# Kernel optimization log

Measured on AMD Instinct MI355X. Metric: run time of the kernel, lower is better.

The kernel has to match this reference:

```python
import jax, jax.numpy as jnp
import numpy as np

B, T, D = 2, 2048, 1024
NH, DH = 16, 64  # inner = NH*DH = D
SCALE_INIT = 0.02


def setup_inputs() -> dict:
    key = jax.random.key(0)
    kx, kq, kk, kv, ko = jax.random.split(key, 5)
    return {
        "x": jax.random.normal(kx, (B, T, D), dtype=jnp.float32),
        "Wq": jax.random.normal(kq, (D, NH * DH), dtype=jnp.float32) * SCALE_INIT,
        "Wk": jax.random.normal(kk, (D, NH * DH), dtype=jnp.float32) * SCALE_INIT,
        "Wv": jax.random.normal(kv, (D, NH * DH), dtype=jnp.float32) * SCALE_INIT,
        "Wo": jax.random.normal(ko, (NH * DH, D), dtype=jnp.float32) * SCALE_INIT,
    }


def reference(x, Wq, Wk, Wv, Wo):
    # x: (B, T, D)
    b, t, _ = x.shape

    def split_heads(h):
        # (B, T, NH*DH) -> (B, NH, T, DH)
        return h.reshape(b, t, NH, DH).transpose(0, 2, 1, 3)

    q = split_heads(x @ Wq)
    k = split_heads(x @ Wk)
    v = split_heads(x @ Wv)

    scale = jnp.asarray(1.0 / np.sqrt(DH), dtype=x.dtype)
    # The per-chunk loop in the original is mathematically equivalent to
    # full causal attention: each query row attends to keys with k_pos <= q_pos.
    scores = jnp.einsum("bhqd,bhkd->bhqk", q, k) * scale  # (B, NH, T, T)
    causal_mask = jnp.arange(t)[None, :] > jnp.arange(t)[:, None]  # k_pos > q_pos
    scores = jnp.where(causal_mask, -jnp.inf, scores)
    attn = jax.nn.softmax(scores, axis=-1)
    attn = jnp.nan_to_num(attn)  # matches torch.nan_to_num (no fully-masked rows in causal case)
    o = jnp.einsum("bhqk,bhkd->bhqd", attn, v)  # (B, NH, T, DH)
    o = o.transpose(0, 2, 1, 3).reshape(b, t, NH * DH)  # merge heads
    return o @ Wo  # (B, T, D)
```

## Files before the change

kernel.cpp:

```cpp
#include <hip/hip_runtime.h>
#include <hip/hip_bf16.h>
#include <string.h>

#define Bsz 2
#define Tsz 2048
#define Dsz 1024
#define NHsz 16
#define Msz (Bsz*Tsz)

typedef unsigned short bfu;
typedef __attribute__((ext_vector_type(8))) short short8;
typedef __attribute__((ext_vector_type(4))) short short4v;
typedef __attribute__((ext_vector_type(4))) float floatx4;

__device__ __forceinline__ bfu f2bf(float f) {
  unsigned int u = __builtin_bit_cast(unsigned int, f);
  u += 0x7fffu + ((u >> 16) & 1u);
  return (bfu)(u >> 16);
}

__device__ __forceinline__ float fexp2(float x) {
#if __has_builtin(__builtin_amdgcn_exp2f)
  return __builtin_amdgcn_exp2f(x);
#else
  return exp2f(x);
#endif
}

__device__ __forceinline__ short4v pack4bf(float a, float b, float c_, float d) {
  __hip_bfloat162 h01 = __float22bfloat162_rn(make_float2(a, b));
  __hip_bfloat162 h23 = __float22bfloat162_rn(make_float2(c_, d));
  uint2 uu;
  memcpy(&uu.x, &h01, 4);
  memcpy(&uu.y, &h23, 4);
  return __builtin_bit_cast(short4v, uu);
}

__device__ __forceinline__ short8 pack8bf(float4 a, float4 b) {
  __hip_bfloat162 h0 = __float22bfloat162_rn(make_float2(a.x, a.y));
  __hip_bfloat162 h1 = __float22bfloat162_rn(make_float2(a.z, a.w));
  __hip_bfloat162 h2 = __float22bfloat162_rn(make_float2(b.x, b.y));
  __hip_bfloat162 h3 = __float22bfloat162_rn(make_float2(b.z, b.w));
  uint4 u;
  memcpy(&u.x, &h0, 4); memcpy(&u.y, &h1, 4);
  memcpy(&u.z, &h2, 4); memcpy(&u.w, &h3, 4);
  return __builtin_bit_cast(short8, u);
}

__device__ __forceinline__ void async16(const void* g, void* l) {
  void* gnc = (void*)g;
  __builtin_amdgcn_global_load_lds((__attribute__((address_space(1))) void*)gnc,
                                   (__attribute__((address_space(3))) void*)l,
                                   16, 0, 0);
}

__global__ __launch_bounds__(256) void xcvt(const float* __restrict__ x, bfu* __restrict__ xb) {
  const size_t i = ((size_t)blockIdx.x * 256 + threadIdx.x) * 8;
  float4 a = *(const float4*)(x + i);
  float4 b = *(const float4*)(x + i + 4);
  *(short8*)(xb + i) = pack8bf(a, b);
}

__global__ __launch_bounds__(256) void transpose_w(const float* __restrict__ W0, const float* __restrict__ W1,
                                                   const float* __restrict__ W2, const float* __restrict__ W3,
                                                   bfu* __restrict__ wt) {
  __shared__ float tile[32][33];
  const float* W = blockIdx.z == 0 ? W0 : blockIdx.z == 1 ? W1 : blockIdx.z == 2 ? W2 : W3;
  const float s = (blockIdx.z == 0) ? 0.18033688011112042f : 1.0f;
  bfu* WT = wt + (size_t)blockIdx.z * Dsz * Dsz;
  int tx = threadIdx.x, ty = threadIdx.y;
  int kb = blockIdx.y * 32, nb = blockIdx.x * 32;
#pragma unroll
  for (int i = 0; i < 4; ++i)
    tile[ty + i*8][tx] = W[(size_t)(kb + ty + i*8) * Dsz + nb + tx];
  __syncthreads();
#pragma unroll
  for (int i = 0; i < 4; ++i)
    WT[(size_t)(nb + ty + i*8) * Dsz + kb + tx] = f2bf(tile[tx][ty + i*8] * s);
}

template <bool F32OUT, int NT>
__global__ __launch_bounds__(256) void gemm128(const bfu* __restrict__ Ain, const bfu* __restrict__ Bt0,
                                               void* __restrict__ C0, int K, int N,
                                               size_t strideB, size_t strideC) {
  constexpr int NJ = NT / 32;
  const int tid = threadIdx.x, wave = tid >> 6, lane = tid & 63;
  const int g = lane >> 4, c = lane & 15;
  const int m0 = blockIdx.y * 128, n0 = blockIdx.x * NT;
  const bfu* Bt = Bt0 + strideB * blockIdx.z;
  __shared__ bfu smem[4096 + NT * 32];
  bfu* As = smem;
  bfu* Bs = smem + 4096;
  floatx4 acc[4][NJ] = {};
  const int srow = lane >> 2, scol = (lane & 3) * 8;
  const bfu* gB = Bt + (size_t)(n0 + srow) * K + scol;
  const int wm = (wave >> 1) * 64, wn = (wave & 1) * (NT / 2);
  const bfu* gA = Ain + (size_t)(m0 + srow) * K + scol;

  for (int k0 = 0; k0 < K; k0 += 32) {
    __syncthreads();
#pragma unroll
    for (int cc = 0; cc < 2; ++cc) {
      const int chunk = wave * 2 + cc;
      async16(gA + (size_t)chunk * 16 * K + k0, &As[chunk * 512]);
    }
#pragma unroll
    for (int cc = 0; cc < NT/64; ++cc) {
      const int chunk = wave * (NT/64) + cc;
      async16(gB + (size_t)chunk * 16 * K + k0, &Bs[chunk * 512]);
    }
    __syncthreads();
    short8 afr[4], bfr[NJ];
#pragma unroll
    for (int t = 0; t < 4; ++t) afr[t] = *(const short8*)&As[(wm + t*16 + c) * 32 + g * 8];
#pragma unroll
    for (int t = 0; t < NJ; ++t) bfr[t] = *(const short8*)&Bs[(wn + t*16 + c) * 32 + g * 8];
#pragma unroll
    for (int i = 0; i < 4; ++i)
#pragma unroll
      for (int j = 0; j < NJ; ++j)
        acc[i][j] = __builtin_amdgcn_mfma_f32_16x16x32_bf16(afr[i], bfr[j], acc[i][j], 0, 0, 0);
  }

  const bool vtrans = (!F32OUT) && (NT == 128) && (blockIdx.z == 2);
  if (vtrans) {
    bfu* vtp = (bfu*)C0 + (size_t)2 * strideC;
#pragma unroll
    for (int p = 0; p < 2; ++p) {
      __syncthreads();
      if ((wave & 1) == p) {
#pragma unroll
        for (int i = 0; i < 4; ++i)
#pragma unroll
          for (int j = 0; j < NJ; ++j) {
            const int nl = j*16 + c;
            const int mg = ((wm + i*16) >> 3) + (g >> 1);
            const int phys = nl * 128 + ((mg ^ (nl & 15)) << 3) + ((g & 1) << 2);
            *(short4v*)&smem[phys] = pack4bf(acc[i][j][0], acc[i][j][1],
                                             acc[i][j][2], acc[i][j][3]);
          }
      }
      __syncthreads();
      const int h_ = (n0 + p * 64) >> 6;
      bfu* dst = vtp + ((size_t)((m0 >> 11) * 16 + h_) * 64) * Tsz + (m0 & 2047);
#pragma unroll
      for (int s = 0; s < 4; ++s) {
        const int nl = s * 16 + (tid >> 4);
        const int me = (tid & 15) << 3;
        const int phys = nl * 128 + (((me >> 3) ^ (nl & 15)) << 3);
        *(short8*)&dst[(size_t)nl * Tsz + me] = *(const short8*)&smem[phys];
      }
    }
    return;
  }

#pragma unroll
  for (int i = 0; i < 4; ++i) {
#pragma unroll
    for (int j = 0; j < NJ; ++j) {
      const int m = m0 + wm + i*16 + g*4;
      const int n = n0 + wn + j*16 + c;
#pragma unroll
      for (int r = 0; r < 4; ++r) {
        float v = acc[i][j][r];
        if (F32OUT) ((float*)C0)[(size_t)(m + r) * N + n] = v;
        else        ((bfu*)C0)[strideC * blockIdx.z + (size_t)(m + r) * N + n] = f2bf(v);
      }
    }
  }
}

__global__ __launch_bounds__(256, 4) void attn_kernel(const bfu* __restrict__ qkv,
                                                      float* __restrict__ op0,
                                                      float* __restrict__ op1,
                                                      float2* __restrict__ ml) {
  const int tid = threadIdx.x, wave = tid >> 6, lane = tid & 63;
  const int g = (lane >> 4) & 3, c = lane & 15, c7 = c & 7;

  const int flat = (int)blockIdx.y * 32 + (int)blockIdx.x;
  const int xcd = flat & 7, r_ = flat >> 3;
  const int ksplit = r_ & 1;
  const int s = (r_ >> 1) & 3, j0 = r_ >> 3;
  const int bh = xcd * 4 + s;
  const int b = bh >> 4, h = bh & 15;

  const size_t hbq = (size_t)b * Tsz * Dsz + h * 64;
  const bfu* Qp = qkv + hbq;
  const bfu* Kp = qkv + (size_t)Msz * Dsz + hbq;
  const bfu* Vt = qkv + (size_t)2 * Msz * Dsz + (size_t)bh * 64 * Tsz;
  float* op = ksplit ? op1 : op0;

  __shared__ bfu Ks[2][64 * 64];
  __shared__ bfu Vs[2][64 * 64];

  const int srow8 = lane >> 3;
  const int soff = ((lane & 7) ^ srow8) << 3;
  const floatx4 z4 = {0.0f, 0.0f, 0.0f, 0.0f};

  for (int hf = 0; hf < 2; ++hf) {
    const int j = hf ? (31 - j0) : j0;
    const int qw = j * 64 + wave * 16;

    short8 bq[2];
#pragma unroll
    for (int kk = 0; kk < 2; ++kk)
      bq[kk] = *(const short8*)(Qp + (size_t)(qw + c) * Dsz + kk * 32 + g * 8);

    floatx4 acc[4] = {};
    float mi = -3.0e38f, li = 0.0f;

    if (ksplit <= j) {
      const bfu* kpp[2]; const bfu* vpp[2];
#pragma unroll
      for (int cc = 0; cc < 2; ++cc) {
        const int ch = wave * 2 + cc;
        kpp[cc] = Kp + (size_t)(ksplit * 64 + ch * 8 + srow8) * Dsz + soff;
        vpp[cc] = Vt + (size_t)(ch * 8 + srow8) * Tsz + ksplit * 64 + soff;
      }

#pragma unroll
      for (int cc = 0; cc < 2; ++cc) {
        const int ch = wave * 2 + cc;
        async16(kpp[cc], &Ks[0][ch * 512]);
        async16(vpp[cc], &Vs[0][ch * 512]);
        kpp[cc] += (size_t)128 * Dsz;
        vpp[cc] += 128;
      }

      int cur = 0;
      for (int kt = ksplit; kt <= j; kt += 2) {
        if (kt + 2 <= j) {
#pragma unroll
          for (int cc = 0; cc < 2; ++cc) {
            const int ch = wave * 2 + cc;
            async16(kpp[cc], &Ks[cur ^ 1][ch * 512]);
            async16(vpp[cc], &Vs[cur ^ 1][ch * 512]);
            kpp[cc] += (size_t)128 * Dsz;
            vpp[cc] += 128;
          }
          asm volatile("s_waitcnt vmcnt(4)" ::: "memory");
        } else {
          asm volatile("s_waitcnt vmcnt(0)" ::: "memory");
        }
        __builtin_amdgcn_s_barrier();
        asm volatile("" ::: "memory");

        const bfu* KsC = &Ks[cur][0];
        const bfu* VsC = &Vs[cur][0];

        floatx4 st[4];
        __builtin_amdgcn_s_setprio(1);
#pragma unroll
        for (int mk = 0; mk < 4; ++mk) {
          const short8 kf = *(const short8*)&KsC[(mk * 16 + c) * 64 + ((g ^ c7) << 3)];
          st[mk] = __builtin_amdgcn_mfma_f32_16x16x32_bf16(kf, bq[0], z4, 0, 0, 0);
        }
#pragma unroll
        for (int mk = 0; mk < 4; ++mk) {
          const short8 kf = *(const short8*)&KsC[(mk * 16 + c) * 64 + (((4 + g) ^ c7) << 3)];
          st[mk] = __builtin_amdgcn_mfma_f32_16x16x32_bf16(kf, bq[1], st[mk], 0, 0, 0);
        }
        __builtin_amdgcn_s_setprio(0);

        if (kt == j) {
#pragma unroll
          for (int mk = 0; mk < 4; ++mk) {
            const int keyb = kt * 64 + mk * 16 + g * 4;
#pragma unroll
            for (int r = 0; r < 4; ++r)
              if (keyb + r > qw + c) st[mk][r] = -1.0e38f;
          }
        }

        float mloc = -3.0e38f;
#pragma unroll
        for (int mk = 0; mk < 4; ++mk)
          mloc = fmaxf(mloc, fmaxf(fmaxf(st[mk][0], st[mk][1]),
                                   fmaxf(st[mk][2], st[mk][3])));
        const bool resc = !__all(mloc <= mi + 8.0f);
        if (resc) {
          float mr = fmaxf(mloc, __shfl_xor(mloc, 16));
          mr = fmaxf(mr, __shfl_xor(mr, 32));
          const float mnew = fmaxf(mi, mr);
          const float alpha = fexp2(mi - mnew);
          li *= alpha;
          mi = mnew;
          float al[4];
#pragma unroll
          for (int rr = 0; rr < 4; ++rr) al[rr] = __shfl(alpha, (lane & 48) | (g * 4 + rr));
#pragma unroll
          for (int nd = 0; nd < 4; ++nd)
#pragma unroll
            for (int rr = 0; rr < 4; ++rr) acc[nd][rr] *= al[rr];
        }
        short4v pa[4];
#pragma unroll
        for (int mk = 0; mk < 4; ++mk) {
          const float p0 = fexp2(st[mk][0] - mi);
          const float p1 = fexp2(st[mk][1] - mi);
          const float p2 = fexp2(st[mk][2] - mi);
          const float p3 = fexp2(st[mk][3] - mi);
          li += (p0 + p1) + (p2 + p3);
          pa[mk] = pack4bf(p0, p1, p2, p3);
        }

        __builtin_amdgcn_s_setprio(1);
#pragma unroll
        for (int mk = 0; mk < 4; ++mk)
#pragma unroll
          for (int nd = 0; nd < 4; ++nd) {
            const short4v vf = *(const short4v*)&VsC[(nd * 16 + c) * 64 +
                ((((mk << 1) + (g >> 1)) ^ c7) << 3) + ((g & 1) << 2)];
            acc[nd] = __builtin_amdgcn_mfma_f32_16x16x16bf16_1k(pa[mk], vf, acc[nd], 0, 0, 0);
          }
        __builtin_amdgcn_s_setprio(0);

        asm volatile("" ::: "memory");
        __builtin_amdgcn_s_barrier();
        asm volatile("" ::: "memory");
        cur ^= 1;
      }
    }

    float lt = li;
    lt += __shfl_xor(lt, 16);
    lt += __shfl_xor(lt, 32);
#pragma unroll
    for (int rr = 0; rr < 4; ++rr) {
      const float lr = __shfl(lt, (lane & 48) | (g * 4 + rr));
      const float inv = lr > 0.0f ? 1.0f / lr : 0.0f;
#pragma unroll
      for (int nd = 0; nd < 4; ++nd)
        op[(size_t)(b * Tsz + qw + g * 4 + rr) * Dsz + h * 64 + nd * 16 + c] =
            acc[nd][rr] * inv;
    }
    if (lane < 16)
      ml[(size_t)ksplit * 65536 + bh * 2048 + qw + c] = make_float2(mi, lt);
  }
}

__global__ __launch_bounds__(256) void merge_split(const float* __restrict__ o0,
                                                   const float* __restrict__ o1,
                                                   const float2* __restrict__ ml,
                                                   bfu* __restrict__ ob) {
  const int idx = blockIdx.x * 256 + threadIdx.x;
  const int row = idx >> 7, ch = idx & 127;
  const int b = row >> 11, q = row & 2047;
  const int bh = b * 16 + (ch >> 3);
  const float2 a0 = ml[bh * 2048 + q];
  const float2 a1 = ml[65536 + bh * 2048 + q];
  const float M = fmaxf(a0.x, a1.x);
  const float w0 = fexp2(a0.x - M) * a0.y;
  const float w1 = fexp2(a1.x - M) * a1.y;
  const float inv = 1.0f / (w0 + w1);
  const float u0 = w0 * inv, u1 = w1 * inv;
  const size_t off = (size_t)row * 1024 + ch * 8;
  float4 p0 = *(const float4*)(o0 + off), q0 = *(const float4*)(o0 + off + 4);
  float4 p1 = *(const float4*)(o1 + off), q1 = *(const float4*)(o1 + off + 4);
  float4 ra, rb;
  ra.x = u0*p0.x + u1*p1.x; ra.y = u0*p0.y + u1*p1.y;
  ra.z = u0*p0.z + u1*p1.z; ra.w = u0*p0.w + u1*p1.w;
  rb.x = u0*q0.x + u1*q1.x; rb.y = u0*q0.y + u1*q1.y;
  rb.z = u0*q0.z + u1*q1.z; rb.w = u0*q0.w + u1*q1.w;
  *(short8*)(ob + off) = pack8bf(ra, rb);
}

extern "C" void kernel_launch(void* const* d_in, const int* in_sizes, int n_in,
                              void* d_out, int out_size, void* d_ws, size_t ws_size,
                              hipStream_t stream) {
  const float* x  = (const float*)d_in[0];
  const float* Wq = (const float*)d_in[1];
  const float* Wk = (const float*)d_in[2];
  const float* Wv = (const float*)d_in[3];
  const float* Wo = (const float*)d_in[4];
  float* out = (float*)d_out;

  bfu* wt    = (bfu*)d_ws;
  bfu* qkv   = wt + (size_t)4 * Dsz * Dsz;
  bfu* obuf  = qkv + (size_t)3 * Msz * Dsz;
  float* op0 = (float*)(obuf + (size_t)Msz * Dsz);
  float* op1 = op0 + (size_t)Msz * Dsz;
  float2* ml = (float2*)(op1 + (size_t)Msz * Dsz);

  transpose_w<<<dim3(32, 32, 4), dim3(32, 8), 0, stream>>>(Wq, Wk, Wv, Wo, wt);
  xcvt<<<dim3(2048), dim3(256), 0, stream>>>(x, obuf);
  gemm128<false, 128><<<dim3(Dsz / 128, Msz / 128, 3), dim3(256), 0, stream>>>(
      obuf, wt, (void*)qkv, Dsz, Dsz, (size_t)Dsz * Dsz, (size_t)Msz * Dsz);
  attn_kernel<<<dim3(32, 32), dim3(256), 0, stream>>>(qkv, op0, op1, ml);
  merge_split<<<dim3(2048), dim3(256), 0, stream>>>(op0, op1, ml, obuf);
  gemm128<true, 64><<<dim3(Dsz / 64, Msz / 128, 1), dim3(256), 0, stream>>>(
      obuf, wt + (size_t)3 * Dsz * Dsz, (void*)out, Dsz, Dsz,
      (size_t)0, (size_t)0);
}
```

Before: 195.9 us.

## Double-buffer GEMM LDS staging with XOR swizzle and fold x conversion into transpose

The bf16 GEMM now keeps two LDS stage buffers and issues the async global-to-LDS loads for the next K step before computing the current one. It waits on vmcnt so the copy overlaps the MFMA work, where before each step loaded and then computed in series. The 16-byte column chunks are XOR-swizzled on both the write and read side to cut LDS bank conflicts. The separate x-to-bf16 conversion kernel becomes an extra z-slice of the weight transpose launch, saving one kernel launch. The costs are doubled LDS per block, which may lower occupancy, and hand-tuned vmcnt counts that must match the number of outstanding loads.

```diff
diff --git a/kernel.cpp b/kernel.cpp
--- a/kernel.cpp
+++ b/kernel.cpp
@@ -54,16 +54,19 @@
                                    16, 0, 0);
 }
 
-__global__ __launch_bounds__(256) void xcvt(const float* __restrict__ x, bfu* __restrict__ xb) {
-  const size_t i = ((size_t)blockIdx.x * 256 + threadIdx.x) * 8;
-  float4 a = *(const float4*)(x + i);
-  float4 b = *(const float4*)(x + i + 4);
-  *(short8*)(xb + i) = pack8bf(a, b);
-}
-
 __global__ __launch_bounds__(256) void transpose_w(const float* __restrict__ W0, const float* __restrict__ W1,
                                                    const float* __restrict__ W2, const float* __restrict__ W3,
-                                                   bfu* __restrict__ wt) {
+                                                   bfu* __restrict__ wt,
+                                                   const float* __restrict__ x, bfu* __restrict__ xb) {
+  if (blockIdx.z == 4) {
+    const int bf = (int)blockIdx.y * 32 + (int)blockIdx.x;
+    const size_t i = ((size_t)bf * 256 + threadIdx.y * 32 + threadIdx.x) * 16;
+    float4 a0 = *(const float4*)(x + i),     a1 = *(const float4*)(x + i + 4);
+    float4 b0 = *(const float4*)(x + i + 8), b1 = *(const float4*)(x + i + 12);
+    *(short8*)(xb + i)     = pack8bf(a0, a1);
+    *(short8*)(xb + i + 8) = pack8bf(b0, b1);
+    return;
+  }
   __shared__ float tile[32][33];
   const float* W = blockIdx.z == 0 ? W0 : blockIdx.z == 1 ? W1 : blockIdx.z == 2 ? W2 : W3;
   const float s = (blockIdx.z == 0) ? 0.18033688011112042f : 1.0f;
@@ -88,42 +91,65 @@
   const int g = lane >> 4, c = lane & 15;
   const int m0 = blockIdx.y * 128, n0 = blockIdx.x * NT;
   const bfu* Bt = Bt0 + strideB * blockIdx.z;
-  __shared__ bfu smem[4096 + NT * 32];
-  bfu* As = smem;
-  bfu* Bs = smem + 4096;
+  __shared__ bfu smem[2][4096 + NT * 32];
   floatx4 acc[4][NJ] = {};
-  const int srow = lane >> 2, scol = (lane & 3) * 8;
+  const int srow = lane >> 2;
+  const int scol = (((lane & 3) ^ ((lane >> 3) & 3)) << 3);
   const bfu* gB = Bt + (size_t)(n0 + srow) * K + scol;
+  const bfu* gA = Ain + (size_t)(m0 + srow) * K + scol;
   const int wm = (wave >> 1) * 64, wn = (wave & 1) * (NT / 2);
-  const bfu* gA = Ain + (size_t)(m0 + srow) * K + scol;
-
-  for (int k0 = 0; k0 < K; k0 += 32) {
-    __syncthreads();
-#pragma unroll
-    for (int cc = 0; cc < 2; ++cc) {
-      const int chunk = wave * 2 + cc;
-      async16(gA + (size_t)chunk * 16 * K + k0, &As[chunk * 512]);
+  const int roct = (g ^ ((c >> 1) & 3)) << 3;
+
+#define STAGE_G(buf, k0)                                                        \
+  {                                                                             \
+    _Pragma("unroll")                                                           \
+    for (int cc = 0; cc < 2; ++cc) {                                            \
+      const int chunk = wave * 2 + cc;                                          \
+      async16(gA + (size_t)chunk * 16 * K + (k0), &smem[buf][chunk * 512]);     \
+    }                                                                           \
+    _Pragma("unroll")                                                           \
+    for (int cc = 0; cc < NT / 64; ++cc) {                                      \
+      const int chunk = wave * (NT / 64) + cc;                                  \
+      async16(gB + (size_t)chunk * 16 * K + (k0), &smem[buf][4096 + chunk * 512]); \
+    }                                                                           \
+  }
+
+  const int NK = K / 32;
+  STAGE_G(0, 0);
+  for (int t = 0; t < NK; ++t) {
+    const int cur = t & 1;
+    if (t + 1 < NK) {
+      STAGE_G(cur ^ 1, (t + 1) * 32);
+      if (NT == 128) asm volatile("s_waitcnt vmcnt(4)" ::: "memory");
+      else           asm volatile("s_waitcnt vmcnt(3)" ::: "memory");
+    } else {
+      asm volatile("s_waitcnt vmcnt(0)" ::: "memory");
     }
-#pragma unroll
-    for (int cc = 0; cc < NT/64; ++cc) {
-      const int chunk = wave * (NT/64) + cc;
-      async16(gB + (size_t)chunk * 16 * K + k0, &Bs[chunk * 512]);
-    }
-    __syncthreads();
+    __builtin_amdgcn_s_barrier();
+    asm volatile("" ::: "memory");
+
+    const bfu* AsC = &smem[cur][0];
+    const bfu* BsC = &smem[cur][4096];
     short8 afr[4], bfr[NJ];
 #pragma unroll
-    for (int t = 0; t < 4; ++t) afr[t] = *(const short8*)&As[(wm + t*16 + c) * 32 + g * 8];
-#pragma unroll
-    for (int t = 0; t < NJ; ++t) bfr[t] = *(const short8*)&Bs[(wn + t*16 + c) * 32 + g * 8];
+    for (int i = 0; i < 4; ++i) afr[i] = *(const short8*)&AsC[(wm + i*16 + c) * 32 + roct];
+#pragma unroll
+    for (int j = 0; j < NJ; ++j) bfr[j] = *(const short8*)&BsC[(wn + j*16 + c) * 32 + roct];
 #pragma unroll
     for (int i = 0; i < 4; ++i)
 #pragma unroll
       for (int j = 0; j < NJ; ++j)
         acc[i][j] = __builtin_amdgcn_mfma_f32_16x16x32_bf16(afr[i], bfr[j], acc[i][j], 0, 0, 0);
-  }
+
+    asm volatile("" ::: "memory");
+    __builtin_amdgcn_s_barrier();
+    asm volatile("" ::: "memory");
+  }
+#undef STAGE_G
 
   const bool vtrans = (!F32OUT) && (NT == 128) && (blockIdx.z == 2);
   if (vtrans) {
+    bfu* sm = &smem[0][0];
     bfu* vtp = (bfu*)C0 + (size_t)2 * strideC;
 #pragma unroll
     for (int p = 0; p < 2; ++p) {
@@ -136,8 +162,8 @@
             const int nl = j*16 + c;
             const int mg = ((wm + i*16) >> 3) + (g >> 1);
             const int phys = nl * 128 + ((mg ^ (nl & 15)) << 3) + ((g & 1) << 2);
-            *(short4v*)&smem[phys] = pack4bf(acc[i][j][0], acc[i][j][1],
-                                             acc[i][j][2], acc[i][j][3]);
+            *(short4v*)&sm[phys] = pack4bf(acc[i][j][0], acc[i][j][1],
+                                           acc[i][j][2], acc[i][j][3]);
           }
       }
       __syncthreads();
@@ -148,7 +174,7 @@
         const int nl = s * 16 + (tid >> 4);
         const int me = (tid & 15) << 3;
         const int phys = nl * 128 + (((me >> 3) ^ (nl & 15)) << 3);
-        *(short8*)&dst[(size_t)nl * Tsz + me] = *(const short8*)&smem[phys];
+        *(short8*)&dst[(size_t)nl * Tsz + me] = *(const short8*)&sm[phys];
       }
     }
     return;
@@ -382,8 +408,7 @@
   float* op1 = op0 + (size_t)Msz * Dsz;
   float2* ml = (float2*)(op1 + (size_t)Msz * Dsz);
 
-  transpose_w<<<dim3(32, 32, 4), dim3(32, 8), 0, stream>>>(Wq, Wk, Wv, Wo, wt);
-  xcvt<<<dim3(2048), dim3(256), 0, stream>>>(x, obuf);
+  transpose_w<<<dim3(32, 32, 5), dim3(32, 8), 0, stream>>>(Wq, Wk, Wv, Wo, wt, x, obuf);
   gemm128<false, 128><<<dim3(Dsz / 128, Msz / 128, 3), dim3(256), 0, stream>>>(
       obuf, wt, (void*)qkv, Dsz, Dsz, (size_t)Dsz * Dsz, (size_t)Msz * Dsz);
   attn_kernel<<<dim3(32, 32), dim3(256), 0, stream>>>(qkv, op0, op1, ml);
```

Result: faster. 185.6 us (-5.3%).
